# Kernel tuning notes

Measured on AMD Instinct MI355X. Metric: run time of the kernel, lower is better.

The kernel has to match this reference:

```python
import jax, jax.numpy as jnp
import numpy as np

# fHOG orientation lookup (cos/sin of k*20 degrees), exactly the hardcoded
# constants used in Felzenszwalb's features.cc / mmcv extract_hog kernel.
UU = jnp.array([1.0000, 0.9397, 0.7660, 0.5000, 0.1736,
                -0.1736, -0.5000, -0.7660, -0.9397], dtype=jnp.float32)
VV = jnp.array([0.0000, 0.3420, 0.6428, 0.8660, 0.9848,
                0.9848, 0.8660, 0.6428, 0.3420], dtype=jnp.float32)
EPS = 1e-4


def _hog(img, sbin):
    B, C, H, W = img.shape
    bh = int(round(H / sbin)); bw = int(round(W / sbin))
    vh, vw = bh * sbin, bw * sbin
    # central differences at pixels (1..visible-2), source index clamped to dim-2
    ys = jnp.clip(jnp.arange(1, vh - 1), 0, H - 2)
    xs = jnp.clip(jnp.arange(1, vw - 1), 0, W - 2)
    dy = img[:, :, ys + 1][:, :, :, xs] - img[:, :, ys - 1][:, :, :, xs]
    dx = img[:, :, ys][:, :, :, xs + 1] - img[:, :, ys][:, :, :, xs - 1]
    v = dx * dx + dy * dy                      # [B,3,hg,wg]
    ch = jnp.argmax(v, axis=1, keepdims=True)  # channel with max gradient energy
    dxs = jnp.take_along_axis(dx, ch, axis=1)[:, 0]
    dys = jnp.take_along_axis(dy, ch, axis=1)[:, 0]
    mag = jnp.sqrt(dxs * dxs + dys * dys)      # [B,hg,wg]
    # snap to one of 18 signed orientations
    dot = UU[None, :, None, None] * dxs[:, None] + VV[None, :, None, None] * dys[:, None]
    best_o = jnp.argmax(jnp.concatenate([dot, -dot], axis=1), axis=1)  # [B,hg,wg]
    # bilinear spatial soft-binning into sbin x sbin cells
    yp = (jnp.arange(1, vh - 1, dtype=img.dtype) + 0.5) / sbin - 0.5
    xp = (jnp.arange(1, vw - 1, dtype=img.dtype) + 0.5) / sbin - 0.5
    iyp = jnp.floor(yp).astype(jnp.int32); ixp = jnp.floor(xp).astype(jnp.int32)
    vy0 = yp - iyp; vx0 = xp - ixp; vy1 = 1.0 - vy0; vx1 = 1.0 - vx0
    hg, wg = vh - 2, vw - 2
    bidx = jnp.arange(B)[:, None, None]
    IY = jnp.broadcast_to(iyp[None, :, None], (B, hg, wg))
    IX = jnp.broadcast_to(ixp[None, None, :], (B, hg, wg))
    WY0 = vy0[None, :, None]; WY1 = vy1[None, :, None]
    WX0 = vx0[None, None, :]; WX1 = vx1[None, None, :]
    hist = jnp.zeros((B, 18, bh, bw), dtype=img.dtype)

    def scat(h, iy, ix, w):
        valid = (iy >= 0) & (iy < bh) & (ix >= 0) & (ix < bw)
        iyc = jnp.clip(iy, 0, bh - 1); ixc = jnp.clip(ix, 0, bw - 1)
        return h.at[bidx, best_o, iyc, ixc].add(jnp.where(valid, w * mag, 0.0))

    hist = scat(hist, IY, IX, WY1 * WX1)
    hist = scat(hist, IY, IX + 1, WY1 * WX0)
    hist = scat(hist, IY + 1, IX, WY0 * WX1)
    hist = scat(hist, IY + 1, IX + 1, WY0 * WX0)
    # cell energy from contrast-insensitive sums
    s = hist[:, :9] + hist[:, 9:]
    norm = jnp.sum(s * s, axis=1)              # [B,bh,bw]
    # 2x2 block sums of norm
    T = norm[:, :-1, :-1] + norm[:, 1:, :-1] + norm[:, :-1, 1:] + norm[:, 1:, 1:]
    n1 = jax.lax.rsqrt(T[:, 1:, 1:] + EPS)[:, None]
    n2 = jax.lax.rsqrt(T[:, :-1, 1:] + EPS)[:, None]
    n3 = jax.lax.rsqrt(T[:, 1:, :-1] + EPS)[:, None]
    n4 = jax.lax.rsqrt(T[:, :-1, :-1] + EPS)[:, None]
    src = hist[:, :, 1:-1, 1:-1]               # [B,18,oh,ow]
    h1 = jnp.minimum(src * n1, 0.2); h2 = jnp.minimum(src * n2, 0.2)
    h3 = jnp.minimum(src * n3, 0.2); h4 = jnp.minimum(src * n4, 0.2)
    f_cs = 0.5 * (h1 + h2 + h3 + h4)           # 18 contrast-sensitive feats
    ss = src[:, :9] + src[:, 9:]
    f_ci = 0.5 * (jnp.minimum(ss * n1, 0.2) + jnp.minimum(ss * n2, 0.2)
                  + jnp.minimum(ss * n3, 0.2) + jnp.minimum(ss * n4, 0.2))
    tex = 0.2357 * jnp.stack([h1.sum(1), h2.sum(1), h3.sum(1), h4.sum(1)], axis=1)
    feat = jnp.concatenate([f_cs, f_ci, tex], axis=1)  # [B,31,oh,ow]
    return jnp.pad(feat, ((0, 0), (0, 0), (1, 1), (1, 1)))


def setup_inputs() -> dict:
    key = jax.random.key(0)
    img = jax.random.uniform(key, (16, 3, 512, 512), dtype=jnp.float32)
    return {"input": img, "sbin": 4}


def reference(input, sbin):
    return _hog(input, sbin)
```

## Files before the change

### kernel.cpp

```cpp
#include <hip/hip_runtime.h>
#include <hip/hip_fp16.h>

#define BATCH 16
#define H 512
#define W 512
#define BH 128
#define BW 128
#define HG 510
#define WG 510
#define PKW 512


__global__ __launch_bounds__(256) void hog_grad(const float* __restrict__ img,
                                                unsigned int* __restrict__ pk)
{
    int gx = blockIdx.x * 64 + threadIdx.x;
    int qy = blockIdx.y * 4 + threadIdx.y;
    int b  = blockIdx.z;
    int x0 = gx * 4;
    int y0 = qy * 4;
    bool edge = (x0 < 508);

    const float* im = img + (size_t)b * 3 * H * W;

    float bv[16], bx[16], by[16];
#pragma unroll
    for (int i = 0; i < 16; i++) { bv[i] = -1.f; bx[i] = 0.f; by[i] = 0.f; }

#pragma unroll
    for (int c = 0; c < 3; c++) {
        const float* base = im + (size_t)c * H * W;
        float Wr[6][6];
#pragma unroll
        for (int j = 0; j < 6; j++) {
            int pr = y0 + j; if (pr > 511) pr = 511;
            const float* rowp = base + (size_t)pr * W + x0;
            float4 a = *(const float4*)rowp;
            Wr[j][0] = a.x; Wr[j][1] = a.y; Wr[j][2] = a.z; Wr[j][3] = a.w;
            if (j >= 1 && j <= 4) {
                if (edge || pr < 511) {
                    float2 f = *(const float2*)(rowp + 4);
                    Wr[j][4] = f.x; Wr[j][5] = f.y;
                } else { Wr[j][4] = 0.f; Wr[j][5] = 0.f; }
            } else {
                Wr[j][4] = edge ? rowp[4] : 0.0f;
                Wr[j][5] = 0.f;
            }
        }
#pragma unroll
        for (int r = 0; r < 4; r++) {
#pragma unroll
            for (int i = 0; i < 4; i++) {
                float dx = __fsub_rn(Wr[r + 1][i + 2], Wr[r + 1][i]);
                float dy = __fsub_rn(Wr[r + 2][i + 1], Wr[r][i + 1]);
                float v = __fadd_rn(__fmul_rn(dx, dx), __fmul_rn(dy, dy));
                int k = r * 4 + i;
                if (v > bv[k]) { bv[k] = v; bx[k] = dx; by[k] = dy; }
            }
        }
    }

    const float uu[9] = {1.0f, 0.9397f, 0.766f, 0.5f, 0.1736f, -0.1736f, -0.5f, -0.766f, -0.9397f};
    const float vv[9] = {0.0f, 0.342f, 0.6428f, 0.866f, 0.9848f, 0.9848f, 0.866f, 0.6428f, 0.342f};

#pragma unroll
    for (int r = 0; r < 4; r++) {
        int y = y0 + r;
        if (y >= HG) break;
        unsigned int pkv[4];
#pragma unroll
        for (int i = 0; i < 4; i++) {
            int k = r * 4 + i;
            float mg = __fsqrt_rn(bv[k]);
            float d[9];
#pragma unroll
            for (int o = 0; o < 9; o++)
                d[o] = __fadd_rn(__fmul_rn(uu[o], bx[k]), __fmul_rn(vv[o], by[k]));
            float best = -1e30f; int bo = 0;
#pragma unroll
            for (int o = 0; o < 9; o++) { if (d[o] > best) { best = d[o]; bo = o; } }
#pragma unroll
            for (int o = 0; o < 9; o++) { float nd = -d[o]; if (nd > best) { best = nd; bo = o + 9; } }
            unsigned int v = (__float_as_uint(mg) & 0xFFFFFFE0u) | (unsigned int)bo;
            pkv[i] = (x0 + i < WG) ? v : 0u;
        }
        uint4 o4 = make_uint4(pkv[0], pkv[1], pkv[2], pkv[3]);
        *(uint4*)(pk + ((size_t)b * HG + y) * PKW + x0) = o4;
    }
}

__global__ __launch_bounds__(256) void hog_hist(const unsigned int* __restrict__ pk,
                                                __half2* __restrict__ hist,
                                                float* __restrict__ nrm)
{
    __shared__ __half2 hl0[9 * 256];
    __shared__ __half2 hl1[9 * 256];
    int cx = threadIdx.x;
    int cy = blockIdx.y * 2 + threadIdx.y;
    int b = blockIdx.z;
    int t = threadIdx.y * 128 + cx;

    const float wt[8] = {0.125f, 0.375f, 0.625f, 0.875f, 0.875f, 0.625f, 0.375f, 0.125f};
    const float wl[4] = {0.0f, 0.125f, 0.375f, 0.625f};
    const float wm[4] = {0.875f, 0.875f, 0.625f, 0.375f};

    const unsigned int* pb = pk + (size_t)b * HG * PKW;
    int ry0 = 4 * cy - 3;
    int xb = 4 * cx;
    int xL = (cx > 0) ? xb - 4 : xb;
    int xR = (cx < 127) ? xb + 4 : xb;
    float wLm = (cx > 0) ? 1.0f : 0.0f;
    float wRm = (cx < 127) ? 1.0f : 0.0f;

    uint4 Lv[8], Mv[8]; unsigned Xv[8]; float wyv[8];
#pragma unroll
    for (int ky = 0; ky < 8; ky++) {
        int ry = ry0 + ky;
        bool ok = (unsigned)ry < (unsigned)HG;
        int ryc = ok ? ry : (ry < 0 ? 0 : HG - 1);
        const unsigned int* row = pb + (size_t)ryc * PKW;
        Lv[ky] = *(const uint4*)(row + xL);
        Mv[ky] = *(const uint4*)(row + xb);
        Xv[ky] = row[xR];
        wyv[ky] = ok ? wt[ky] : 0.0f;
    }

    const __half2 z2 = __halves2half2(__ushort_as_half(0), __ushort_as_half(0));
#pragma unroll
    for (int o = 0; o < 9; o++) { hl0[o * 256 + t] = z2; hl1[o * 256 + t] = z2; }

#define ACC(B, P, WW) { unsigned _p = (P); unsigned _o = _p & 31u;                         \
        __half _hv = __float2half((WW) * __uint_as_float(_p & 0xFFFFFFE0u));               \
        bool _lo = _o < 9u; unsigned _o9 = _lo ? _o : _o - 9u;                             \
        __half2 _ad = _lo ? __halves2half2(_hv, __ushort_as_half(0))                       \
                          : __halves2half2(__ushort_as_half(0), _hv);                      \
        B[_o9 * 256 + t] = __hadd2(B[_o9 * 256 + t], _ad); }

#pragma unroll
    for (int ky = 0; ky < 8; ky++) {
        float wy = wyv[ky];
        uint4 L = Lv[ky], M = Mv[ky];
        ACC(hl0, L.y, (wy * wl[1]) * wLm);
        ACC(hl1, L.z, (wy * wl[2]) * wLm);
        ACC(hl0, L.w, (wy * wl[3]) * wLm);
        ACC(hl1, M.x, wy * wm[0]);
        ACC(hl0, M.y, wy * wm[1]);
        ACC(hl1, M.z, wy * wm[2]);
        ACC(hl0, M.w, wy * wm[3]);
        ACC(hl1, Xv[ky], (wy * 0.125f) * wRm);
    }
#undef ACC

    float s = 0.0f;
#pragma unroll
    for (int o = 0; o < 9; o++) {
        __half2 hh = __hadd2(hl0[o * 256 + t], hl1[o * 256 + t]);
        hist[(((size_t)b * 9 + o) * BH + cy) * BW + cx] = hh;
        float2 f = __half22float2(hh);
        float ss = f.x + f.y;
        s += ss * ss;
    }
    nrm[((size_t)b * BH + cy) * BW + cx] = s;
}

__global__ __launch_bounds__(256) void hog_feat(const __half2* __restrict__ hist,
                                                const float* __restrict__ nrm,
                                                float* __restrict__ out)
{
    int tx = threadIdx.x;
    int oy = blockIdx.y * 8 + threadIdx.y;
    int b  = blockIdx.z;
    int cx0 = tx * 4;

    if (oy == 0 || oy == BH - 1) {
        float4 z4 = make_float4(0.f, 0.f, 0.f, 0.f);
#pragma unroll
        for (int c = 0; c < 31; c++)
            *(float4*)(out + (((size_t)b * 31 + c) * BH + oy) * BW + cx0) = z4;
        return;
    }

    float v1[4], v2[4], v3[4], v4[4];
    {
        const float* nb = nrm + (size_t)b * BH * BW;
        float nn[3][6];
#pragma unroll
        for (int r = 0; r < 3; r++) {
            const float* rp = nb + (size_t)(oy - 1 + r) * BW + cx0;
#pragma unroll
            for (int j = 0; j < 6; j++) nn[r][j] = rp[j - 1];
        }
#pragma unroll
        for (int i = 0; i < 4; i++) {
            float T11 = nn[1][i+1] + nn[2][i+1] + nn[1][i+2] + nn[2][i+2];
            float T01 = nn[0][i+1] + nn[1][i+1] + nn[0][i+2] + nn[1][i+2];
            float T10 = nn[1][i]   + nn[2][i]   + nn[1][i+1] + nn[2][i+1];
            float T00 = nn[0][i]   + nn[1][i]   + nn[0][i+1] + nn[1][i+1];
            v1[i] = 1.0f / __fsqrt_rn(T11 + 1e-4f);
            v2[i] = 1.0f / __fsqrt_rn(T01 + 1e-4f);
            v3[i] = 1.0f / __fsqrt_rn(T10 + 1e-4f);
            v4[i] = 1.0f / __fsqrt_rn(T00 + 1e-4f);
        }
    }

    float h[4][18];
#pragma unroll
    for (int o = 0; o < 9; o++) {
        uint4 q = *(const uint4*)(hist + (((size_t)b * 9 + o) * BH + oy) * BW + cx0);
        unsigned vs[4] = {q.x, q.y, q.z, q.w};
#pragma unroll
        for (int i = 0; i < 4; i++) {
            float2 f = __half22float2(*(__half2*)&vs[i]);
            h[i][o] = f.x; h[i][o + 9] = f.y;
        }
    }

    bool msk[4];
#pragma unroll
    for (int i = 0; i < 4; i++) { int cxi = cx0 + i; msk[i] = (cxi >= 1 && cxi <= 126); }

    float t1[4] = {0,0,0,0}, t2[4] = {0,0,0,0}, t3[4] = {0,0,0,0}, t4[4] = {0,0,0,0};
    float* ob = out + ((size_t)b * 31) * BH * BW + (size_t)oy * BW + cx0;

#pragma unroll
    for (int o = 0; o < 18; o++) {
        float st[4];
#pragma unroll
        for (int i = 0; i < 4; i++) {
            float s = h[i][o];
            float a1 = fminf(s * v1[i], 0.2f);
            float a2 = fminf(s * v2[i], 0.2f);
            float a3 = fminf(s * v3[i], 0.2f);
            float a4 = fminf(s * v4[i], 0.2f);
            t1[i] += a1; t2[i] += a2; t3[i] += a3; t4[i] += a4;
            st[i] = msk[i] ? 0.5f * (a1 + a2 + a3 + a4) : 0.f;
        }
        *(float4*)(ob + (size_t)o * BH * BW) = make_float4(st[0], st[1], st[2], st[3]);
    }
#pragma unroll
    for (int o = 0; o < 9; o++) {
        float st[4];
#pragma unroll
        for (int i = 0; i < 4; i++) {
            float ss = h[i][o] + h[i][o + 9];
            float a1 = fminf(ss * v1[i], 0.2f);
            float a2 = fminf(ss * v2[i], 0.2f);
            float a3 = fminf(ss * v3[i], 0.2f);
            float a4 = fminf(ss * v4[i], 0.2f);
            st[i] = msk[i] ? 0.5f * (a1 + a2 + a3 + a4) : 0.f;
        }
        *(float4*)(ob + (size_t)(18 + o) * BH * BW) = make_float4(st[0], st[1], st[2], st[3]);
    }
    {
        float s1[4], s2[4], s3[4], s4[4];
#pragma unroll
        for (int i = 0; i < 4; i++) {
            s1[i] = msk[i] ? 0.2357f * t1[i] : 0.f;
            s2[i] = msk[i] ? 0.2357f * t2[i] : 0.f;
            s3[i] = msk[i] ? 0.2357f * t3[i] : 0.f;
            s4[i] = msk[i] ? 0.2357f * t4[i] : 0.f;
        }
        *(float4*)(ob + (size_t)27 * BH * BW) = make_float4(s1[0], s1[1], s1[2], s1[3]);
        *(float4*)(ob + (size_t)28 * BH * BW) = make_float4(s2[0], s2[1], s2[2], s2[3]);
        *(float4*)(ob + (size_t)29 * BH * BW) = make_float4(s3[0], s3[1], s3[2], s3[3]);
        *(float4*)(ob + (size_t)30 * BH * BW) = make_float4(s4[0], s4[1], s4[2], s4[3]);
    }
}

extern "C" void kernel_launch(void* const* d_in, const int* in_sizes, int n_in,
                              void* d_out, int out_size, void* d_ws, size_t ws_size,
                              hipStream_t stream)
{
    const float* img = (const float*)d_in[0];
    float* out = (float*)d_out;
    char* ws = (char*)d_ws;

    unsigned int* pk = (unsigned int*)ws;
    __half2* hist    = (__half2*)(ws + 16715776);
    float* nrm       = (float*)(ws + 26152960);

    dim3 b1(64, 4, 1), g1(2, 32, BATCH);
    hog_grad<<<g1, b1, 0, stream>>>(img, pk);

    dim3 b2(128, 2, 1), g2(1, BH / 2, BATCH);
    hog_hist<<<g2, b2, 0, stream>>>(pk, hist, nrm);

    dim3 b3(32, 8, 1), g3(1, BH / 8, BATCH);
    hog_feat<<<g3, b3, 0, stream>>>(hist, nrm, out);
}
```

Measured before the change: 117.3 us.

## Fuse gradient and histogram kernels via shared-memory packed tile

Merges the gradient/orientation kernel and the histogram kernel into one. Each block computes packed magnitude and orientation for a 68x72 pixel halo tile into LDS, then bins 16x16 cells from LDS. This removes the global round trip of the packed gradient buffer (about 16 MB) and one kernel launch. In exchange, halo pixels are recomputed at tile borders and the block uses more LDS, which may limit occupancy.

```diff
diff --git a/kernel.cpp b/kernel.cpp
--- a/kernel.cpp
+++ b/kernel.cpp
@@ -8,126 +8,87 @@
 #define BW 128
 #define HG 510
 #define WG 510
-#define PKW 512
-
-
-__global__ __launch_bounds__(256) void hog_grad(const float* __restrict__ img,
-                                                unsigned int* __restrict__ pk)
+
+
+__global__ __launch_bounds__(256, 4) void hog_gradhist(const float* __restrict__ img,
+                                                       __half2* __restrict__ hist,
+                                                       float* __restrict__ nrm)
 {
-    int gx = blockIdx.x * 64 + threadIdx.x;
-    int qy = blockIdx.y * 4 + threadIdx.y;
-    int b  = blockIdx.z;
-    int x0 = gx * 4;
-    int y0 = qy * 4;
-    bool edge = (x0 < 508);
+    __shared__ unsigned int pk[68 * 72];
+    __shared__ __half2 hl0[9 * 256];
+    __shared__ __half2 hl1[9 * 256];
+
+    const int t = threadIdx.x;
+    const int b = blockIdx.z;
+    const int cx0 = blockIdx.x * 16;
+    const int cy0 = blockIdx.y * 16;
+    const int gr0 = 4 * cy0 - 3;
+    const int gc0 = 4 * cx0 - 4;
 
     const float* im = img + (size_t)b * 3 * H * W;
-
-    float bv[16], bx[16], by[16];
-#pragma unroll
-    for (int i = 0; i < 16; i++) { bv[i] = -1.f; bx[i] = 0.f; by[i] = 0.f; }
-
-#pragma unroll
-    for (int c = 0; c < 3; c++) {
-        const float* base = im + (size_t)c * H * W;
-        float Wr[6][6];
-#pragma unroll
-        for (int j = 0; j < 6; j++) {
-            int pr = y0 + j; if (pr > 511) pr = 511;
-            const float* rowp = base + (size_t)pr * W + x0;
-            float4 a = *(const float4*)rowp;
-            Wr[j][0] = a.x; Wr[j][1] = a.y; Wr[j][2] = a.z; Wr[j][3] = a.w;
-            if (j >= 1 && j <= 4) {
-                if (edge || pr < 511) {
-                    float2 f = *(const float2*)(rowp + 4);
-                    Wr[j][4] = f.x; Wr[j][5] = f.y;
-                } else { Wr[j][4] = 0.f; Wr[j][5] = 0.f; }
-            } else {
-                Wr[j][4] = edge ? rowp[4] : 0.0f;
-                Wr[j][5] = 0.f;
-            }
-        }
-#pragma unroll
-        for (int r = 0; r < 4; r++) {
-#pragma unroll
-            for (int i = 0; i < 4; i++) {
-                float dx = __fsub_rn(Wr[r + 1][i + 2], Wr[r + 1][i]);
-                float dy = __fsub_rn(Wr[r + 2][i + 1], Wr[r][i + 1]);
-                float v = __fadd_rn(__fmul_rn(dx, dx), __fmul_rn(dy, dy));
-                int k = r * 4 + i;
-                if (v > bv[k]) { bv[k] = v; bx[k] = dx; by[k] = dy; }
-            }
-        }
-    }
 
     const float uu[9] = {1.0f, 0.9397f, 0.766f, 0.5f, 0.1736f, -0.1736f, -0.5f, -0.766f, -0.9397f};
     const float vv[9] = {0.0f, 0.342f, 0.6428f, 0.866f, 0.9848f, 0.9848f, 0.866f, 0.6428f, 0.342f};
 
-#pragma unroll
-    for (int r = 0; r < 4; r++) {
-        int y = y0 + r;
-        if (y >= HG) break;
-        unsigned int pkv[4];
-#pragma unroll
-        for (int i = 0; i < 4; i++) {
-            int k = r * 4 + i;
-            float mg = __fsqrt_rn(bv[k]);
-            float d[9];
-#pragma unroll
-            for (int o = 0; o < 9; o++)
-                d[o] = __fadd_rn(__fmul_rn(uu[o], bx[k]), __fmul_rn(vv[o], by[k]));
-            float best = -1e30f; int bo = 0;
-#pragma unroll
-            for (int o = 0; o < 9; o++) { if (d[o] > best) { best = d[o]; bo = o; } }
-#pragma unroll
-            for (int o = 0; o < 9; o++) { float nd = -d[o]; if (nd > best) { best = nd; bo = o + 9; } }
-            unsigned int v = (__float_as_uint(mg) & 0xFFFFFFE0u) | (unsigned int)bo;
-            pkv[i] = (x0 + i < WG) ? v : 0u;
-        }
-        uint4 o4 = make_uint4(pkv[0], pkv[1], pkv[2], pkv[3]);
-        *(uint4*)(pk + ((size_t)b * HG + y) * PKW + x0) = o4;
-    }
-}
-
-__global__ __launch_bounds__(256) void hog_hist(const unsigned int* __restrict__ pk,
-                                                __half2* __restrict__ hist,
-                                                float* __restrict__ nrm)
-{
-    __shared__ __half2 hl0[9 * 256];
-    __shared__ __half2 hl1[9 * 256];
-    int cx = threadIdx.x;
-    int cy = blockIdx.y * 2 + threadIdx.y;
-    int b = blockIdx.z;
-    int t = threadIdx.y * 128 + cx;
-
-    const float wt[8] = {0.125f, 0.375f, 0.625f, 0.875f, 0.875f, 0.625f, 0.375f, 0.125f};
-    const float wl[4] = {0.0f, 0.125f, 0.375f, 0.625f};
-    const float wm[4] = {0.875f, 0.875f, 0.625f, 0.375f};
-
-    const unsigned int* pb = pk + (size_t)b * HG * PKW;
-    int ry0 = 4 * cy - 3;
-    int xb = 4 * cx;
-    int xL = (cx > 0) ? xb - 4 : xb;
-    int xR = (cx < 127) ? xb + 4 : xb;
-    float wLm = (cx > 0) ? 1.0f : 0.0f;
-    float wRm = (cx < 127) ? 1.0f : 0.0f;
-
-    uint4 Lv[8], Mv[8]; unsigned Xv[8]; float wyv[8];
-#pragma unroll
-    for (int ky = 0; ky < 8; ky++) {
-        int ry = ry0 + ky;
-        bool ok = (unsigned)ry < (unsigned)HG;
-        int ryc = ok ? ry : (ry < 0 ? 0 : HG - 1);
-        const unsigned int* row = pb + (size_t)ryc * PKW;
-        Lv[ky] = *(const uint4*)(row + xL);
-        Mv[ky] = *(const uint4*)(row + xb);
-        Xv[ky] = row[xR];
-        wyv[ky] = ok ? wt[ky] : 0.0f;
-    }
-
     const __half2 z2 = __halves2half2(__ushort_as_half(0), __ushort_as_half(0));
 #pragma unroll
     for (int o = 0; o < 9; o++) { hl0[o * 256 + t] = z2; hl1[o * 256 + t] = z2; }
+
+    for (int it = 0; it < 5; ++it) {
+        int s = it * 256 + t;
+        if (s >= 68 * 18) break;
+        int r = s / 18;
+        int q = s - r * 18;
+        int gr = gr0 + r;
+        int gc = gc0 + 4 * q;
+        unsigned int pkv[4] = {0u, 0u, 0u, 0u};
+        if (gr >= 0 && gr < HG && gc >= 0 && gc < WG) {
+            int o2 = (gc == 508) ? 2 : 4;
+            float bv[4] = {-1.f, -1.f, -1.f, -1.f}, bxv[4], byv[4];
+            const float* p0 = im + (size_t)gr * W + gc;
+#pragma unroll
+            for (int c = 0; c < 3; c++) {
+                const float* pu = p0 + (size_t)c * H * W;
+                const float* pm = pu + W;
+                const float* pd = pm + W;
+                float4 a0 = *(const float4*)pu;  float2 e0 = *(const float2*)(pu + o2);
+                float4 a1 = *(const float4*)pm;  float2 e1 = *(const float2*)(pm + o2);
+                float4 a2 = *(const float4*)pd;  float2 e2 = *(const float2*)(pd + o2);
+                float u_[6] = {a0.x, a0.y, a0.z, a0.w, e0.x, e0.y};
+                float m_[6] = {a1.x, a1.y, a1.z, a1.w, e1.x, e1.y};
+                float d_[6] = {a2.x, a2.y, a2.z, a2.w, e2.x, e2.y};
+#pragma unroll
+                for (int i = 0; i < 4; i++) {
+                    float dx = __fsub_rn(m_[i + 2], m_[i]);
+                    float dy = __fsub_rn(d_[i + 1], u_[i + 1]);
+                    float v = __fadd_rn(__fmul_rn(dx, dx), __fmul_rn(dy, dy));
+                    if (v > bv[i]) { bv[i] = v; bxv[i] = dx; byv[i] = dy; }
+                }
+            }
+#pragma unroll
+            for (int i = 0; i < 4; i++) {
+                if (gc + i < WG) {
+                    float mg = __fsqrt_rn(bv[i]);
+                    float dt[9];
+#pragma unroll
+                    for (int o = 0; o < 9; o++)
+                        dt[o] = __fadd_rn(__fmul_rn(uu[o], bxv[i]), __fmul_rn(vv[o], byv[i]));
+                    float best = -1e30f; int bo = 0;
+#pragma unroll
+                    for (int o = 0; o < 9; o++) { if (dt[o] > best) { best = dt[o]; bo = o; } }
+#pragma unroll
+                    for (int o = 0; o < 9; o++) { float nd = -dt[o]; if (nd > best) { best = nd; bo = o + 9; } }
+                    pkv[i] = (__float_as_uint(mg) & 0xFFFFFFE0u) | (unsigned int)bo;
+                }
+            }
+        }
+        *(uint4*)&pk[r * 72 + 4 * q] = make_uint4(pkv[0], pkv[1], pkv[2], pkv[3]);
+    }
+
+    __syncthreads();
+
+    const int cxL = t & 15, cyL = t >> 4;
+    const float wt8[8] = {0.125f, 0.375f, 0.625f, 0.875f, 0.875f, 0.625f, 0.375f, 0.125f};
 
 #define ACC(B, P, WW) { unsigned _p = (P); unsigned _o = _p & 31u;                         \
         __half _hv = __float2half((WW) * __uint_as_float(_p & 0xFFFFFFE0u));               \
@@ -138,19 +99,23 @@
 
 #pragma unroll
     for (int ky = 0; ky < 8; ky++) {
-        float wy = wyv[ky];
-        uint4 L = Lv[ky], M = Mv[ky];
-        ACC(hl0, L.y, (wy * wl[1]) * wLm);
-        ACC(hl1, L.z, (wy * wl[2]) * wLm);
-        ACC(hl0, L.w, (wy * wl[3]) * wLm);
-        ACC(hl1, M.x, wy * wm[0]);
-        ACC(hl0, M.y, wy * wm[1]);
-        ACC(hl1, M.z, wy * wm[2]);
-        ACC(hl0, M.w, wy * wm[3]);
-        ACC(hl1, Xv[ky], (wy * 0.125f) * wRm);
+        const unsigned int* row = &pk[(4 * cyL + ky) * 72];
+        uint4 L = *(const uint4*)&row[4 * cxL];
+        uint4 M = *(const uint4*)&row[4 * cxL + 4];
+        unsigned int X = row[4 * cxL + 8];
+        float wy = wt8[ky];
+        ACC(hl0, L.y, wy * 0.125f);
+        ACC(hl1, L.z, wy * 0.375f);
+        ACC(hl0, L.w, wy * 0.625f);
+        ACC(hl1, M.x, wy * 0.875f);
+        ACC(hl0, M.y, wy * 0.875f);
+        ACC(hl1, M.z, wy * 0.625f);
+        ACC(hl0, M.w, wy * 0.375f);
+        ACC(hl1, X,   wy * 0.125f);
     }
 #undef ACC
 
+    const int cx = cx0 + cxL, cy = cy0 + cyL;
     float s = 0.0f;
 #pragma unroll
     for (int o = 0; o < 9; o++) {
@@ -275,15 +240,11 @@
     float* out = (float*)d_out;
     char* ws = (char*)d_ws;
 
-    unsigned int* pk = (unsigned int*)ws;
-    __half2* hist    = (__half2*)(ws + 16715776);
-    float* nrm       = (float*)(ws + 26152960);
-
-    dim3 b1(64, 4, 1), g1(2, 32, BATCH);
-    hog_grad<<<g1, b1, 0, stream>>>(img, pk);
-
-    dim3 b2(128, 2, 1), g2(1, BH / 2, BATCH);
-    hog_hist<<<g2, b2, 0, stream>>>(pk, hist, nrm);
+    __half2* hist = (__half2*)ws;
+    float* nrm    = (float*)(ws + 9437184);
+
+    dim3 b1(256, 1, 1), g1(BW / 16, BH / 16, BATCH);
+    hog_gradhist<<<g1, b1, 0, stream>>>(img, hist, nrm);
 
     dim3 b3(32, 8, 1), g3(1, BH / 8, BATCH);
     hog_feat<<<g3, b3, 0, stream>>>(hist, nrm, out);
```

Result: slower. 121.5 us (+3.6%).
